# Optimization experiments

Measured on AMD Instinct MI355X. Metric: run time of the kernel, lower is better.

The kernel has to match this reference:

```python
import jax, jax.numpy as jnp
import numpy as np

# PLN channel layout per 51-channel group:
#   0      : existence prob
#   1:21   : 20 class probs
#   21:23  : xy offsets (unused in get_poss)
#   23:37  : x-link probs (14)
#   37:51  : y-link probs (14)

def _get_poss(cor, cen):
    # cor, cen: [N, 51, 14, 14]  (spatial index i = ix*14+iy)
    # out[n,c,ix,iy,sx,sy] = 0.5 * cor0[n,ix,iy]*cen0[n,sx,sy]
    #   * corC[n,c,ix,iy]*cenC[n,c,sx,sy]
    #   * cor[n,23+sx,ix,iy]*cor[n,37+sy,ix,iy]
    #   * cen[n,23+ix,sx,sy]*cen[n,37+iy,sx,sy]
    A = (cor[:, 0:1] * cor[:, 1:21])[:, :, :, :, None, None]          # [N,20,ix,iy,1,1]
    B = (cen[:, 0:1] * cen[:, 1:21])[:, :, None, None, :, :]          # [N,20,1,1,sx,sy]
    Lcx = jnp.transpose(cor[:, 23:37], (0, 2, 3, 1))[:, None, :, :, :, None]  # [N,1,ix,iy,sx,1]
    Lcy = jnp.transpose(cor[:, 37:51], (0, 2, 3, 1))[:, None, :, :, None, :]  # [N,1,ix,iy,1,sy]
    Lsx = cen[:, 23:37][:, None, :, None, :, :]                       # [N,1,ix,1,sx,sy]
    Lsy = cen[:, 37:51][:, None, None, :, :, :]                       # [N,1,1,iy,sx,sy]
    return 0.5 * A * B * Lcx * Lcy * Lsx * Lsy                        # [N,20,14,14,14,14]


def setup_inputs() -> dict:
    key = jax.random.key(0)
    inference = jax.random.uniform(key, (32, 204, 14, 14), dtype=jnp.float32)
    return {"inference": inference}


def reference(inference):
    N = inference.shape[0]
    g = inference.reshape(N, 4, 51, 14, 14)
    corner1, corner2, center1, center2 = g[:, 0], g[:, 1], g[:, 2], g[:, 3]
    p1 = _get_poss(corner1, center1)
    p2 = _get_poss(corner2, center1)
    p3 = _get_poss(corner1, center2)
    p4 = _get_poss(corner2, center2)
    return (p1, p2, p3, p4)
```

## Files before the change

kernel.cpp:

```cpp
#include <hip/hip_runtime.h>


#define S_PER 24586240u
#define TSTRIDE (51 * 196)
#define N_STRIDE (204 * 196)
#define QSTEP (5u * 196u * 196u)

__global__ __launch_bounds__(256) void plnet_kernel(const float* __restrict__ in,
                                                    float* __restrict__ out) {
    __shared__ float sK1[20], sK2[20];
    __shared__ float sM11[196], sM21[196], sM12[196], sM22[196];

    const unsigned b  = blockIdx.x;
    const unsigned n  = b / 196u;
    const unsigned pc = b % 196u;
    const unsigned d2 = pc / 14u;
    const unsigned d3 = pc % 14u;

    const float* g    = in + (size_t)n * N_STRIDE;
    const float* cor1 = g;
    const float* cor2 = g + TSTRIDE;
    const float* cen1 = g + 2 * TSTRIDE;
    const float* cen2 = g + 3 * TSTRIDE;

    const unsigned tid = threadIdx.x;

    if (tid < 196u) {
        const unsigned ps = tid;
        const unsigned d4 = ps / 14u, d5 = ps % 14u;
        const float e1 = cen1[ps] * cen1[(23u + d2) * 196u + ps] * cen1[(37u + d3) * 196u + ps];
        const float e2 = cen2[ps] * cen2[(23u + d2) * 196u + ps] * cen2[(37u + d3) * 196u + ps];
        const float f1 = cor1[(23u + d4) * 196u + pc] * cor1[(37u + d5) * 196u + pc];
        const float f2 = cor2[(23u + d4) * 196u + pc] * cor2[(37u + d5) * 196u + pc];
        sM11[ps] = f1 * e1;
        sM21[ps] = f2 * e1;
        sM12[ps] = f1 * e2;
        sM22[ps] = f2 * e2;
    } else if (tid < 216u) {
        const unsigned q = tid - 196u;
        sK1[q] = 0.5f * cor1[pc] * cor1[(1u + q) * 196u + pc];
        sK2[q] = 0.5f * cor2[pc] * cor2[(1u + q) * 196u + pc];
    }
    __syncthreads();

    if (tid < 245u) {
        const unsigned qg = tid / 49u;
        const unsigned f  = tid - qg * 49u;
        const unsigned e  = 4u * f;

        const float4 m11 = *(const float4*)&sM11[e];
        const float4 m21 = *(const float4*)&sM21[e];
        const float4 m12 = *(const float4*)&sM12[e];
        const float4 m22 = *(const float4*)&sM22[e];

        size_t base = ((size_t)(n * 20u + qg) * 196u + pc) * 196u + e;
        const float* px1 = &cen1[(1u + qg) * 196u + e];
        const float* px2 = &cen2[(1u + qg) * 196u + e];

#pragma unroll
        for (unsigned k = 0; k < 4u; ++k) {
            const unsigned q = qg + 5u * k;
            const float4 x1 = *(const float4*)px1;
            const float4 x2 = *(const float4*)px2;
            const float k1 = sK1[q], k2 = sK2[q];

            float4* o1 = (float4*)(out + base);
            float4* o2 = (float4*)(out + (size_t)S_PER + base);
            float4* o3 = (float4*)(out + 2u * (size_t)S_PER + base);
            float4* o4 = (float4*)(out + 3u * (size_t)S_PER + base);

            *o1 = make_float4(k1 * m11.x * x1.x, k1 * m11.y * x1.y,
                              k1 * m11.z * x1.z, k1 * m11.w * x1.w);
            *o2 = make_float4(k2 * m21.x * x1.x, k2 * m21.y * x1.y,
                              k2 * m21.z * x1.z, k2 * m21.w * x1.w);
            *o3 = make_float4(k1 * m12.x * x2.x, k1 * m12.y * x2.y,
                              k1 * m12.z * x2.z, k1 * m12.w * x2.w);
            *o4 = make_float4(k2 * m22.x * x2.x, k2 * m22.y * x2.y,
                              k2 * m22.z * x2.z, k2 * m22.w * x2.w);

            base += (size_t)QSTEP;
            px1  += 5u * 196u;
            px2  += 5u * 196u;
        }
    }
}

extern "C" void kernel_launch(void* const* d_in, const int* in_sizes, int n_in,
                              void* d_out, int out_size, void* d_ws, size_t ws_size,
                              hipStream_t stream) {
    const float* in = (const float*)d_in[0];
    float* out = (float*)d_out;
    dim3 grid(32 * 196);
    dim3 block(256);
    plnet_kernel<<<grid, block, 0, stream>>>(in, out);
}
```

Measured before the change: 106.5 us.

## Remap blocks to (n,class,ix) for contiguous output chunks per block

```diff
diff --git a/kernel.cpp b/kernel.cpp
--- a/kernel.cpp
+++ b/kernel.cpp
@@ -4,18 +4,19 @@
 #define S_PER 24586240u
 #define TSTRIDE (51 * 196)
 #define N_STRIDE (204 * 196)
-#define QSTEP (5u * 196u * 196u)
 
 __global__ __launch_bounds__(256) void plnet_kernel(const float* __restrict__ in,
                                                     float* __restrict__ out) {
-    __shared__ float sK1[20], sK2[20];
-    __shared__ float sM11[196], sM21[196], sM12[196], sM22[196];
+    __shared__ __align__(16) float sT1[196];
+    __shared__ __align__(16) float sT2[196];
+    __shared__ float sA1[196], sA2[196];
+    __shared__ float sB1[196], sB2[196];
 
     const unsigned b  = blockIdx.x;
-    const unsigned n  = b / 196u;
-    const unsigned pc = b % 196u;
-    const unsigned d2 = pc / 14u;
-    const unsigned d3 = pc % 14u;
+    const unsigned d2 = b % 14u;
+    const unsigned nq = b / 14u;
+    const unsigned q  = nq % 20u;
+    const unsigned n  = nq / 20u;
 
     const float* g    = in + (size_t)n * N_STRIDE;
     const float* cor1 = g;
@@ -27,61 +28,56 @@
 
     if (tid < 196u) {
         const unsigned ps = tid;
-        const unsigned d4 = ps / 14u, d5 = ps % 14u;
-        const float e1 = cen1[ps] * cen1[(23u + d2) * 196u + ps] * cen1[(37u + d3) * 196u + ps];
-        const float e2 = cen2[ps] * cen2[(23u + d2) * 196u + ps] * cen2[(37u + d3) * 196u + ps];
-        const float f1 = cor1[(23u + d4) * 196u + pc] * cor1[(37u + d5) * 196u + pc];
-        const float f2 = cor2[(23u + d4) * 196u + pc] * cor2[(37u + d5) * 196u + pc];
-        sM11[ps] = f1 * e1;
-        sM21[ps] = f2 * e1;
-        sM12[ps] = f1 * e2;
-        sM22[ps] = f2 * e2;
-    } else if (tid < 216u) {
-        const unsigned q = tid - 196u;
-        sK1[q] = 0.5f * cor1[pc] * cor1[(1u + q) * 196u + pc];
-        sK2[q] = 0.5f * cor2[pc] * cor2[(1u + q) * 196u + pc];
+        sT1[ps] = cen1[ps] * cen1[(1u + q) * 196u + ps] * cen1[(23u + d2) * 196u + ps];
+        sT2[ps] = cen2[ps] * cen2[(1u + q) * 196u + ps] * cen2[(23u + d2) * 196u + ps];
+        const unsigned d3 = ps / 14u;
+        const unsigned k  = ps - d3 * 14u;
+        const unsigned pc = d2 * 14u + d3;
+        const float k1 = 0.5f * cor1[pc] * cor1[(1u + q) * 196u + pc];
+        const float k2 = 0.5f * cor2[pc] * cor2[(1u + q) * 196u + pc];
+        sA1[ps] = k1 * cor1[(23u + k) * 196u + pc];
+        sA2[ps] = k2 * cor2[(23u + k) * 196u + pc];
+        sB1[ps] = cor1[(37u + k) * 196u + pc];
+        sB2[ps] = cor2[(37u + k) * 196u + pc];
     }
     __syncthreads();
 
-    if (tid < 245u) {
-        const unsigned qg = tid / 49u;
-        const unsigned f  = tid - qg * 49u;
+    const size_t chunk = ((size_t)(n * 20u + q) * 196u + d2 * 14u) * 196u;
+    float4* o1 = (float4*)(out + chunk);
+    float4* o2 = (float4*)(out + (size_t)S_PER + chunk);
+    float4* o3 = (float4*)(out + 2u * (size_t)S_PER + chunk);
+    float4* o4 = (float4*)(out + 3u * (size_t)S_PER + chunk);
+
+    for (unsigned c = tid; c < 686u; c += 256u) {
+        const unsigned d3 = c / 49u;
+        const unsigned f  = c - d3 * 49u;
         const unsigned e  = 4u * f;
 
-        const float4 m11 = *(const float4*)&sM11[e];
-        const float4 m21 = *(const float4*)&sM21[e];
-        const float4 m12 = *(const float4*)&sM12[e];
-        const float4 m22 = *(const float4*)&sM22[e];
+        const float4 t1 = *(const float4*)&sT1[e];
+        const float4 t2 = *(const float4*)&sT2[e];
+        const float4 v1 = *(const float4*)&cen1[(37u + d3) * 196u + e];
+        const float4 v2 = *(const float4*)&cen2[(37u + d3) * 196u + e];
 
-        size_t base = ((size_t)(n * 20u + qg) * 196u + pc) * 196u + e;
-        const float* px1 = &cen1[(1u + qg) * 196u + e];
-        const float* px2 = &cen2[(1u + qg) * 196u + e];
+        const float4 G1 = make_float4(t1.x * v1.x, t1.y * v1.y, t1.z * v1.z, t1.w * v1.w);
+        const float4 G2 = make_float4(t2.x * v2.x, t2.y * v2.y, t2.z * v2.z, t2.w * v2.w);
 
+        unsigned d4 = e / 14u;
+        unsigned d5 = e - d4 * 14u;
+        float F1[4], F2[4];
 #pragma unroll
-        for (unsigned k = 0; k < 4u; ++k) {
-            const unsigned q = qg + 5u * k;
-            const float4 x1 = *(const float4*)px1;
-            const float4 x2 = *(const float4*)px2;
-            const float k1 = sK1[q], k2 = sK2[q];
+        for (int l = 0; l < 4; ++l) {
+            F1[l] = sA1[d3 * 14u + d4] * sB1[d3 * 14u + d5];
+            F2[l] = sA2[d3 * 14u + d4] * sB2[d3 * 14u + d5];
+            ++d5;
+            const unsigned carry = (d5 == 14u);
+            d4 += carry;
+            d5 = carry ? 0u : d5;
+        }
 
-            float4* o1 = (float4*)(out + base);
-            float4* o2 = (float4*)(out + (size_t)S_PER + base);
-            float4* o3 = (float4*)(out + 2u * (size_t)S_PER + base);
-            float4* o4 = (float4*)(out + 3u * (size_t)S_PER + base);
-
-            *o1 = make_float4(k1 * m11.x * x1.x, k1 * m11.y * x1.y,
-                              k1 * m11.z * x1.z, k1 * m11.w * x1.w);
-            *o2 = make_float4(k2 * m21.x * x1.x, k2 * m21.y * x1.y,
-                              k2 * m21.z * x1.z, k2 * m21.w * x1.w);
-            *o3 = make_float4(k1 * m12.x * x2.x, k1 * m12.y * x2.y,
-                              k1 * m12.z * x2.z, k1 * m12.w * x2.w);
-            *o4 = make_float4(k2 * m22.x * x2.x, k2 * m22.y * x2.y,
-                              k2 * m22.z * x2.z, k2 * m22.w * x2.w);
-
-            base += (size_t)QSTEP;
-            px1  += 5u * 196u;
-            px2  += 5u * 196u;
-        }
+        o1[c] = make_float4(F1[0] * G1.x, F1[1] * G1.y, F1[2] * G1.z, F1[3] * G1.w);
+        o2[c] = make_float4(F2[0] * G1.x, F2[1] * G1.y, F2[2] * G1.z, F2[3] * G1.w);
+        o3[c] = make_float4(F1[0] * G2.x, F1[1] * G2.y, F1[2] * G2.z, F1[3] * G2.w);
+        o4[c] = make_float4(F2[0] * G2.x, F2[1] * G2.y, F2[2] * G2.z, F2[3] * G2.w);
     }
 }
 
@@ -90,7 +86,7 @@
                               hipStream_t stream) {
     const float* in = (const float*)d_in[0];
     float* out = (float*)d_out;
-    dim3 grid(32 * 196);
+    dim3 grid(32 * 20 * 14);
     dim3 block(256);
     plnet_kernel<<<grid, block, 0, stream>>>(in, out);
 }
```

Result: faster. 89.52 us (-15.9%).
